# Kernel tuning notes

Measured on AMD Instinct MI355X. Metric: run time of the kernel, lower is better.

Reference implementation:

```python
import jax, jax.numpy as jnp
import numpy as np

NUM_OBJ = 32
OBJ_DIM = 128
MSG_W = 256
FIN_W = 256
BATCH = 256
BN_EPS = 1e-5
NEG_SLOPE = 0.01


def _linear_init(key, fan_in, fan_out):
    # torch nn.Linear default: U(-1/sqrt(fan_in), 1/sqrt(fan_in))
    kw, kb = jax.random.split(key)
    bound = 1.0 / np.sqrt(fan_in)
    w = jax.random.uniform(kw, (fan_out, fan_in), jnp.float32, -bound, bound)
    b = jax.random.uniform(kb, (fan_out,), jnp.float32, -bound, bound)
    return w, b


def setup_inputs() -> dict:
    key = jax.random.key(0)
    ks = jax.random.split(key, 8)
    state = jax.random.normal(ks[0], (BATCH, NUM_OBJ, OBJ_DIM), jnp.float32)
    edges = jax.random.randint(ks[1], (BATCH, NUM_OBJ * NUM_OBJ), 0, 2).astype(jnp.float32)
    msg_w1, msg_b1 = _linear_init(ks[2], OBJ_DIM * 2, MSG_W)
    msg_w2, msg_b2 = _linear_init(ks[3], MSG_W, OBJ_DIM)
    fin_w1, fin_b1 = _linear_init(ks[4], OBJ_DIM * 2, FIN_W)
    fin_w2, fin_b2 = _linear_init(ks[5], FIN_W, OBJ_DIM)
    msg_gamma = jnp.ones((MSG_W,), jnp.float32)
    msg_beta = jnp.zeros((MSG_W,), jnp.float32)
    fin_gamma = jnp.ones((FIN_W,), jnp.float32)
    fin_beta = jnp.zeros((FIN_W,), jnp.float32)
    return {
        "state": state, "edges": edges,
        "msg_w1": msg_w1, "msg_b1": msg_b1, "msg_gamma": msg_gamma, "msg_beta": msg_beta,
        "msg_w2": msg_w2, "msg_b2": msg_b2,
        "fin_w1": fin_w1, "fin_b1": fin_b1, "fin_gamma": fin_gamma, "fin_beta": fin_beta,
        "fin_w2": fin_w2, "fin_b2": fin_b2,
    }


def _batchnorm_train(x, gamma, beta):
    # training-mode BatchNorm1d: batch stats over rows, biased variance
    mean = jnp.mean(x, axis=0)
    var = jnp.mean(jnp.square(x - mean), axis=0)
    return (x - mean) * jax.lax.rsqrt(var + BN_EPS) * gamma + beta


def _mlp(x, w1, b1, gamma, beta, w2, b2):
    h = x @ w1.T + b1
    h = _batchnorm_train(h, gamma, beta)
    h = jnp.where(h >= 0, h, NEG_SLOPE * h)  # LeakyReLU
    return h @ w2.T + b2


def reference(state, edges, msg_w1, msg_b1, msg_gamma, msg_beta, msg_w2, msg_b2,
              fin_w1, fin_b1, fin_gamma, fin_beta, fin_w2, fin_b2):
    B, n, d = state.shape
    src = jnp.repeat(jnp.arange(n), n)   # [n*n]
    tgt = jnp.tile(jnp.arange(n), n)     # [n*n]
    sources = state[:, src]              # [B, n*n, d]
    targets = state[:, tgt]              # [B, n*n, d]
    e = edges[:, :, None]                # [B, n*n, 1]
    need = jnp.concatenate([sources * e, targets * e], axis=2)  # [B, n*n, 2d]
    msgs = _mlp(need.reshape(-1, 2 * d), msg_w1, msg_b1, msg_gamma, msg_beta, msg_w2, msg_b2)
    agg = jnp.sum(msgs.reshape(B, n, n, d), axis=2)  # sum over inner edge group
    sm = jnp.concatenate([state, agg], axis=2).reshape(-1, 2 * d)
    out = _mlp(sm, fin_w1, fin_b1, fin_gamma, fin_beta, fin_w2, fin_b2)
    return out.reshape(B, n, d)
```

## Files before the change

### kernel.cpp

```cpp
#include <hip/hip_runtime.h>

#define NOBJ   32
#define DIM    128
#define HW     256
#define R1     8192
#define NPAIR  262144
#define BN_EPS 1e-5f

typedef unsigned short u16;
typedef unsigned int   u32;
typedef __attribute__((ext_vector_type(8))) short bf16x8;
typedef __attribute__((ext_vector_type(4))) float f32x4;
typedef __attribute__((ext_vector_type(4))) unsigned short u16x4;
typedef __attribute__((ext_vector_type(4))) unsigned int u32x4;

__device__ __forceinline__ u16 f2bf(float f) {
    union { float f; unsigned u; } v; v.f = f;
    unsigned r = v.u + 0x7fffu + ((v.u >> 16) & 1u);
    return (u16)(r >> 16);
}
__device__ __forceinline__ float bf2f(u16 u) {
    union { unsigned u; float f; } v; v.u = ((unsigned)u) << 16; return v.f;
}
__device__ __forceinline__ u16x4 cvt4(float4 v) {
    u16x4 r;
    r[0] = f2bf(v.x); r[1] = f2bf(v.y); r[2] = f2bf(v.z); r[3] = f2bf(v.w);
    return r;
}
__device__ __forceinline__ bf16x8 cvt8_f32(const float* p) {
    f32x4 v0 = *(const f32x4*)p, v1 = *(const f32x4*)(p + 4);
    bf16x8 r;
    #pragma unroll
    for (int k = 0; k < 4; ++k) {
        r[k]     = (short)f2bf(v0[k]);
        r[4 + k] = (short)f2bf(v1[k]);
    }
    return r;
}
__device__ __forceinline__ bf16x8 cvt8_bn(const float* p, const float* a, const float* d) {
    f32x4 v0 = *(const f32x4*)p, v1 = *(const f32x4*)(p + 4);
    f32x4 a0 = *(const f32x4*)a, a1 = *(const f32x4*)(a + 4);
    f32x4 d0 = *(const f32x4*)d, d1 = *(const f32x4*)(d + 4);
    bf16x8 r;
    #pragma unroll
    for (int k = 0; k < 4; ++k) {
        float x0 = fmaf(a0[k], v0[k], d0[k]); x0 = fmaxf(x0, 0.01f * x0);
        float x1 = fmaf(a1[k], v1[k], d1[k]); x1 = fmaxf(x1, 0.01f * x1);
        r[k]     = (short)f2bf(x0);
        r[4 + k] = (short)f2bf(x1);
    }
    return r;
}

__global__ __launch_bounds__(256) void prep_kernel(
    const float* __restrict__ w1, const float4* __restrict__ w2,
    const float4* __restrict__ fw1, const float4* __restrict__ fw2,
    u16x4* __restrict__ W1b, u16x4* __restrict__ W2b,
    u16x4* __restrict__ FW1b, u16x4* __restrict__ FW2b,
    f32x4* __restrict__ sums)
{
    int g = blockIdx.x * 256 + threadIdx.x;
    if (g < 16384) {
        const int o = g * 4, n = o >> 7, k = o & 127;
        const float4 v = *(const float4*)(w1 + (n < 256 ? n * 256 + k
                                                        : (n - 256) * 256 + 128 + k));
        W1b[g] = cvt4(v); return;
    }
    g -= 16384;
    if (g < 8192) { W2b[g] = cvt4(w2[g]); return; }
    g -= 8192;
    if (g < 16384) { FW1b[g] = cvt4(fw1[g]); return; }
    g -= 16384;
    if (g < 8192) { FW2b[g] = cvt4(fw2[g]); return; }
    g -= 8192;
    if (g < 264) { const f32x4 z = {}; sums[g] = z; }
}

__global__ __launch_bounds__(512) void pq_stats(
    const float* __restrict__ state, const u16* __restrict__ W1b,
    const float* __restrict__ edges, const float* __restrict__ b1,
    u16* __restrict__ PQb, u16* __restrict__ Ab, float* __restrict__ EQf,
    float* __restrict__ sums)
{
    __shared__ float Pls[32 * 256];
    __shared__ float Qls[33 * 256];
    __shared__ float redA[8 * 256];
    __shared__ float redB[8 * 256];
    __shared__ u32 masks[32];
    __shared__ __align__(16) unsigned char list8[32 * 32];
    __shared__ float cdf[32];

    const int b    = blockIdx.x;
    const int t    = threadIdx.x;
    const int lane = t & 63;
    const int w    = t >> 6;
    const int lr   = lane & 15;
    const int lk   = (lane >> 4) * 8;
    const int c0   = lane * 4;

    if (t < 256) ((u32*)list8)[t] = 0x20202020u;
    if (t < 64) { const f32x4 z = {}; *(f32x4*)&Qls[32 * 256 + t * 4] = z; }

    const int il_t = t >> 5;
    const int j_t  = t & 31;
    const float ev0 = edges[(size_t)b * 1024 + il_t * 32 + j_t];
    const float ev1 = edges[(size_t)b * 1024 + (il_t + 16) * 32 + j_t];

    const int col0 = w * 64;
    f32x4 acc[2][4] = {};
    #pragma unroll
    for (int ks = 0; ks < 4; ++ks) {
        const int kabs = ks * 32 + lk;
        bf16x8 af[2];
        #pragma unroll
        for (int rf = 0; rf < 2; ++rf)
            af[rf] = cvt8_f32(state + (size_t)(b * 32 + rf * 16 + lr) * 128 + kabs);
        if (w == 0) {
            #pragma unroll
            for (int rf = 0; rf < 2; ++rf)
                *(bf16x8*)(Ab + (size_t)(b * 32 + rf * 16 + lr) * 128 + kabs) = af[rf];
        }
        #pragma unroll
        for (int cf = 0; cf < 4; ++cf) {
            const bf16x8 bf = *(const bf16x8*)(W1b + (size_t)(col0 + cf * 16 + lr) * 128 + kabs);
            #pragma unroll
            for (int rf = 0; rf < 2; ++rf)
                acc[rf][cf] = __builtin_amdgcn_mfma_f32_16x16x32_bf16(af[rf], bf, acc[rf][cf], 0, 0, 0);
        }
    }
    #pragma unroll
    for (int rf = 0; rf < 2; ++rf)
        #pragma unroll
        for (int cf = 0; cf < 4; ++cf) {
            const int col = col0 + cf * 16 + lr;
            #pragma unroll
            for (int r = 0; r < 4; ++r) {
                const int row = rf * 16 + (lane >> 4) * 4 + r;
                const u16 u = f2bf(acc[rf][cf][r]);
                PQb[(size_t)(b * 32 + row) * 512 + col] = u;
                const float fv = bf2f(u);
                if (w < 4) Pls[row * 256 + col]         = fv;
                else       Qls[row * 256 + (col - 256)] = fv;
            }
        }
    __syncthreads();

    {
        const unsigned long long bal0 = __ballot(ev0 != 0.f);
        const u32 m0 = (lane < 32) ? (u32)bal0 : (u32)(bal0 >> 32);
        if (ev0 != 0.f)
            list8[il_t * 32 + __popc(m0 & ((1u << j_t) - 1u))] = (unsigned char)j_t;
        if (j_t == 0) masks[il_t] = m0;
        const unsigned long long bal1 = __ballot(ev1 != 0.f);
        const u32 m1 = (lane < 32) ? (u32)bal1 : (u32)(bal1 >> 32);
        if (ev1 != 0.f)
            list8[(il_t + 16) * 32 + __popc(m1 & ((1u << j_t) - 1u))] = (unsigned char)j_t;
        if (j_t == 0) masks[il_t + 16] = m1;
    }
    __syncthreads();

    if (t < 32) {
        u32 cnt = 0;
        #pragma unroll
        for (int i = 0; i < 32; ++i) cnt += (masks[i] >> t) & 1u;
        cdf[t] = (float)cnt;
    }
    if (t == 0) {
        int tot = 0;
        #pragma unroll
        for (int i = 0; i < 32; ++i) tot += __popc(masks[i]);
        atomicAdd(&sums[512], (float)tot);
    }

    const f32x4 b14 = *(const f32x4*)(b1 + c0);
    f32x4 sumA = {}, sumB = {};

    #pragma unroll
    for (int ii = 0; ii < 4; ++ii) {
        const int il = w * 4 + ii;
        const int n1 = __popc(masks[il]);
        const int npad = (n1 + 3) & ~3;
        const float frd = (float)n1;
        f32x4 eq = {};
        const u32x4 l0 = *(const u32x4*)(list8 + il * 32);
        const u32x4 l1 = *(const u32x4*)(list8 + il * 32 + 16);
        const u32 wbuf[8] = {l0[0], l0[1], l0[2], l0[3], l1[0], l1[1], l1[2], l1[3]};
        #pragma unroll
        for (int wi = 0; wi < 8; ++wi) {
            if (wi * 4 >= npad) break;
            const u32 w4 = wbuf[wi];
            #pragma unroll
            for (int kb = 0; kb < 4; ++kb) {
                const int j = (w4 >> (kb * 8)) & 0xff;
                const f32x4 q = *(const f32x4*)&Qls[j * 256 + c0];
                #pragma unroll
                for (int k = 0; k < 4; ++k) eq[k] += q[k];
            }
        }
        *(f32x4*)(EQf + (size_t)(b * 32 + il) * 256 + c0) = eq;
        const f32x4 p4 = *(const f32x4*)&Pls[il * 256 + c0];
        #pragma unroll
        for (int k = 0; k < 4; ++k) {
            const float pb = p4[k] + b14[k];
            sumA[k] += frd * pb + eq[k];
            sumB[k] = fmaf(frd * pb + 2.f * eq[k], pb, sumB[k]);
        }
    }
    __syncthreads();

    #pragma unroll
    for (int jj = 0; jj < 4; ++jj) {
        const int j = w * 4 + jj;
        const float cdj = cdf[j];
        const f32x4 q = *(const f32x4*)&Qls[j * 256 + c0];
        #pragma unroll
        for (int k = 0; k < 4; ++k) sumB[k] = fmaf(cdj * q[k], q[k], sumB[k]);
    }
    *(f32x4*)&redA[w * 256 + c0] = sumA;
    *(f32x4*)&redB[w * 256 + c0] = sumB;
    __syncthreads();
    if (t < 256) {
        float a = 0.f, bb = 0.f;
        #pragma unroll
        for (int ww = 0; ww < 8; ++ww) {
            a  += redA[ww * 256 + t];
            bb += redB[ww * 256 + t];
        }
        atomicAdd(&sums[t], a);
        atomicAdd(&sums[256 + t], bb);
    }
}

__global__ __launch_bounds__(256) void s_agg_kernel(
    const u16* __restrict__ PQb, const float* __restrict__ edges,
    const float* __restrict__ EQf, const float* __restrict__ sums,
    const float* __restrict__ gamma, const float* __restrict__ beta,
    const float* __restrict__ b1,
    const u16* __restrict__ W2b, const float* __restrict__ b2,
    u16* __restrict__ aggb)
{
    __shared__ float Qls[33 * 256];
    __shared__ u16 Ssb[16 * 256];
    __shared__ __align__(16) unsigned char list8[16 * 32];
    __shared__ int n1s[16];

    const int b    = blockIdx.x;
    const int i0   = blockIdx.y * 16;
    const int t    = threadIdx.x;
    const int lane = t & 63;
    const int w    = t >> 6;
    const int lr   = lane & 15;
    const int lk   = (lane >> 4) * 8;
    const int c0   = lane * 4;

    const float Etot = sums[512];
    const float nz   = (float)NPAIR - Etot;
    const float invN = 1.f / (float)NPAIR;
    const f32x4 s1  = *(const f32x4*)(sums + c0);
    const f32x4 s2  = *(const f32x4*)(sums + 256 + c0);
    const f32x4 g4  = *(const f32x4*)(gamma + c0);
    const f32x4 be4 = *(const f32x4*)(beta + c0);
    const f32x4 b14 = *(const f32x4*)(b1 + c0);
    f32x4 a4, d4, ld4;
    #pragma unroll
    for (int k = 0; k < 4; ++k) {
        const float mean = (s1[k] + nz * b14[k]) * invN;
        const float ms   = (s2[k] + nz * b14[k] * b14[k]) * invN;
        const float var  = fmaf(-mean, mean, ms);
        a4[k]  = g4[k] * rsqrtf(var + BN_EPS);
        d4[k]  = fmaf(b14[k] - mean, a4[k], be4[k]);
        ld4[k] = fmaxf(d4[k], 0.01f * d4[k]);
    }

    #pragma unroll
    for (int it = 0; it < 8; ++it) {
        const int row = w + it * 4;
        const u16x4 qu = *(const u16x4*)(PQb + (size_t)(b * 32 + row) * 512 + 256 + c0);
        f32x4 q;
        #pragma unroll
        for (int k = 0; k < 4; ++k) q[k] = a4[k] * bf2f(qu[k]);
        *(f32x4*)&Qls[row * 256 + c0] = q;
    }
    if (t < 64) { const f32x4 z = {}; *(f32x4*)&Qls[32 * 256 + t * 4] = z; }
    if (t < 128) ((u32*)list8)[t] = 0x20202020u;

    const int il_t = t >> 5;
    const int j_t  = t & 31;
    const float ev0 = edges[(size_t)b * 1024 + (i0 + il_t) * 32 + j_t];
    const float ev1 = edges[(size_t)b * 1024 + (i0 + 8 + il_t) * 32 + j_t];
    __syncthreads();

    {
        const unsigned long long bal0 = __ballot(ev0 != 0.f);
        const u32 m0 = (lane < 32) ? (u32)bal0 : (u32)(bal0 >> 32);
        if (ev0 != 0.f)
            list8[il_t * 32 + __popc(m0 & ((1u << j_t) - 1u))] = (unsigned char)j_t;
        if (j_t == 0) n1s[il_t] = __popc(m0);
        const unsigned long long bal1 = __ballot(ev1 != 0.f);
        const u32 m1 = (lane < 32) ? (u32)bal1 : (u32)(bal1 >> 32);
        if (ev1 != 0.f)
            list8[(8 + il_t) * 32 + __popc(m1 & ((1u << j_t) - 1u))] = (unsigned char)j_t;
        if (j_t == 0) n1s[8 + il_t] = __popc(m1);
    }
    __syncthreads();

    #pragma unroll
    for (int ii = 0; ii < 4; ++ii) {
        const int il = 4 * w + ii;
        const int gi = b * 32 + i0 + il;
        const int n1 = n1s[il];
        const int npad = (n1 + 3) & ~3;
        const float frd = (float)n1;
        const float fz = (float)(32 - n1);
        const float fp = (float)(npad - n1);
        const u16x4 pu = *(const u16x4*)(PQb + (size_t)gi * 512 + c0);
        const f32x4 eq4 = *(const f32x4*)(EQf + (size_t)gi * 256 + c0);
        f32x4 ap, absacc;
        #pragma unroll
        for (int k = 0; k < 4; ++k) {
            ap[k] = fmaf(a4[k], bf2f(pu[k]), d4[k]);
            absacc[k] = -fp * fabsf(ap[k]);
        }
        const u32x4 l0 = *(const u32x4*)(list8 + il * 32);
        const u32x4 l1 = *(const u32x4*)(list8 + il * 32 + 16);
        const u32 wbuf[8] = {l0[0], l0[1], l0[2], l0[3], l1[0], l1[1], l1[2], l1[3]};
        #pragma unroll
        for (int wi = 0; wi < 8; ++wi) {
            if (wi * 4 >= npad) break;
            const u32 w4 = wbuf[wi];
            #pragma unroll
            for (int kb = 0; kb < 4; ++kb) {
                const int j = (w4 >> (kb * 8)) & 0xff;
                const f32x4 q = *(const f32x4*)&Qls[j * 256 + c0];
                #pragma unroll
                for (int k = 0; k < 4; ++k)
                    absacc[k] += fabsf(ap[k] + q[k]);
            }
        }
        u16x4 o;
        #pragma unroll
        for (int k = 0; k < 4; ++k) {
            const float lin = fmaf(frd, ap[k], a4[k] * eq4[k]);
            const float S = fmaf(fz, ld4[k], fmaf(0.505f, lin, 0.495f * absacc[k]));
            o[k] = f2bf(S);
        }
        const int off = (lane * 8) ^ ((il & 7) << 4);
        *(u16x4*)((char*)Ssb + il * 512 + off) = o;
    }
    __syncthreads();

    const int colw = w * 32;
    f32x4 acc2[2] = {};
    #pragma unroll
    for (int ks = 0; ks < 8; ++ks) {
        const int rdoff = (ks * 64 + (lane >> 4) * 16) ^ ((lr & 7) << 4);
        const bf16x8 afr = *(const bf16x8*)((const char*)Ssb + lr * 512 + rdoff);
        #pragma unroll
        for (int cf = 0; cf < 2; ++cf) {
            const bf16x8 bfr = *(const bf16x8*)(W2b + (size_t)(colw + cf * 16 + lr) * 256 + ks * 32 + lk);
            acc2[cf] = __builtin_amdgcn_mfma_f32_16x16x32_bf16(afr, bfr, acc2[cf], 0, 0, 0);
        }
    }
    #pragma unroll
    for (int cf = 0; cf < 2; ++cf) {
        const int col = colw + cf * 16 + lr;
        const float bv = (float)NOBJ * b2[col];
        #pragma unroll
        for (int r = 0; r < 4; ++r) {
            const int rowl = (lane >> 4) * 4 + r;
            aggb[(size_t)(b * 32 + i0 + rowl) * 128 + col] = f2bf(acc2[cf][r] + bv);
        }
    }
}

__global__ __launch_bounds__(256) void h2_gemm(
    const u16* __restrict__ Ab, const u16* __restrict__ aggb,
    const u16* __restrict__ FW1b, const float* __restrict__ fb1,
    float* __restrict__ H2, float* __restrict__ sums2)
{
    __shared__ float sred[64];
    const int lane = threadIdx.x & 63;
    const int wave = threadIdx.x >> 6;
    const int row0 = blockIdx.y * 64 + wave * 16;
    const int col0 = blockIdx.x * 32;
    const int lr = lane & 15;
    const int lk = (lane >> 4) * 8;

    f32x4 acc[2] = {};
    #pragma unroll
    for (int ks = 0; ks < 8; ++ks) {
        const int kabs = ks * 32 + lk;
        const bf16x8 af = (kabs < 128)
            ? *(const bf16x8*)(Ab   + (size_t)(row0 + lr) * 128 + kabs)
            : *(const bf16x8*)(aggb + (size_t)(row0 + lr) * 128 + (kabs - 128));
        #pragma unroll
        for (int cf = 0; cf < 2; ++cf) {
            const bf16x8 bf = *(const bf16x8*)(FW1b + (size_t)(col0 + cf * 16 + lr) * 256 + kabs);
            acc[cf] = __builtin_amdgcn_mfma_f32_16x16x32_bf16(af, bf, acc[cf], 0, 0, 0);
        }
    }

    if (threadIdx.x < 64) sred[threadIdx.x] = 0.f;
    __syncthreads();
    #pragma unroll
    for (int cf = 0; cf < 2; ++cf) {
        const int col = col0 + cf * 16 + lr;
        const float bv = fb1[col];
        float s = 0.f, ss = 0.f;
        #pragma unroll
        for (int r = 0; r < 4; ++r) {
            const int row = row0 + (lane >> 4) * 4 + r;
            const float v = acc[cf][r] + bv;
            H2[(size_t)row * 256 + col] = v;
            s += v;
            ss = fmaf(v, v, ss);
        }
        atomicAdd(&sred[cf * 16 + lr], s);
        atomicAdd(&sred[32 + cf * 16 + lr], ss);
    }
    __syncthreads();
    if (threadIdx.x < 32) {
        atomicAdd(&sums2[col0 + threadIdx.x], sred[threadIdx.x]);
        atomicAdd(&sums2[256 + col0 + threadIdx.x], sred[32 + threadIdx.x]);
    }
}

__global__ __launch_bounds__(256) void out_gemm(
    const float* __restrict__ H2, const u16* __restrict__ FW2b,
    const float* __restrict__ fb2, const float* __restrict__ sums2,
    const float* __restrict__ gamma, const float* __restrict__ beta,
    float* __restrict__ out)
{
    __shared__ float adl[512];
    const int t = threadIdx.x;
    {
        const float invN = 1.f / (float)R1;
        const float mean = sums2[t] * invN;
        const float var  = fmaf(-mean, mean, sums2[256 + t] * invN);
        const float a    = gamma[t] * rsqrtf(var + BN_EPS);
        adl[t]       = a;
        adl[256 + t] = fmaf(-mean, a, beta[t]);
    }
    __syncthreads();

    const int lane = t & 63;
    const int wave = t >> 6;
    const int row0 = blockIdx.y * 64 + wave * 16;
    const int col0 = blockIdx.x * 32;
    const int lr = lane & 15;
    const int lk = (lane >> 4) * 8;

    f32x4 acc[2] = {};
    #pragma unroll
    for (int ks = 0; ks < 8; ++ks) {
        const int kabs = ks * 32 + lk;
        const bf16x8 af = cvt8_bn(H2 + (size_t)(row0 + lr) * 256 + kabs,
                                  adl + kabs, adl + 256 + kabs);
        #pragma unroll
        for (int cf = 0; cf < 2; ++cf) {
            const bf16x8 bf = *(const bf16x8*)(FW2b + (size_t)(col0 + cf * 16 + lr) * 256 + kabs);
            acc[cf] = __builtin_amdgcn_mfma_f32_16x16x32_bf16(af, bf, acc[cf], 0, 0, 0);
        }
    }
    #pragma unroll
    for (int cf = 0; cf < 2; ++cf) {
        const int col = col0 + cf * 16 + lr;
        const float bv = fb2[col];
        #pragma unroll
        for (int r = 0; r < 4; ++r) {
            const int row = row0 + (lane >> 4) * 4 + r;
            out[(size_t)row * 128 + col] = acc[cf][r] + bv;
        }
    }
}

extern "C" void kernel_launch(void* const* d_in, const int* in_sizes, int n_in,
                              void* d_out, int out_size, void* d_ws, size_t ws_size,
                              hipStream_t stream)
{
    const float* state     = (const float*)d_in[0];
    const float* edges     = (const float*)d_in[1];
    const float* msg_w1    = (const float*)d_in[2];
    const float* msg_b1    = (const float*)d_in[3];
    const float* msg_gamma = (const float*)d_in[4];
    const float* msg_beta  = (const float*)d_in[5];
    const float* msg_w2    = (const float*)d_in[6];
    const float* msg_b2    = (const float*)d_in[7];
    const float* fin_w1    = (const float*)d_in[8];
    const float* fin_b1    = (const float*)d_in[9];
    const float* fin_gamma = (const float*)d_in[10];
    const float* fin_beta  = (const float*)d_in[11];
    const float* fin_w2    = (const float*)d_in[12];
    const float* fin_b2    = (const float*)d_in[13];

    char* w = (char*)d_ws;
    u16*   PQb  = (u16*)(w);
    u16*   Ab   = (u16*)(w + 8388608);
    u16*   aggb = (u16*)(w + 10485760);
    float* H2   = (float*)(w + 12582912);
    float* EQf  = (float*)(w + 20971520);
    u16*   W1b  = (u16*)(w + 29360128);
    u16*   W2b  = (u16*)(w + 29491200);
    u16*   FW1b = (u16*)(w + 29556736);
    u16*   FW2b = (u16*)(w + 29687808);
    float* sums = (float*)(w + 29753344);
    float* sums2 = sums + 544;

    prep_kernel<<<195, 256, 0, stream>>>(
        msg_w1, (const float4*)msg_w2, (const float4*)fin_w1, (const float4*)fin_w2,
        (u16x4*)W1b, (u16x4*)W2b, (u16x4*)FW1b, (u16x4*)FW2b, (f32x4*)sums);

    pq_stats<<<256, 512, 0, stream>>>(state, W1b, edges, msg_b1,
                                      PQb, Ab, EQf, sums);

    s_agg_kernel<<<dim3(256, 2), 256, 0, stream>>>(
        PQb, edges, EQf, sums, msg_gamma, msg_beta, msg_b1, W2b, msg_b2, aggb);

    h2_gemm<<<dim3(8, 128), 256, 0, stream>>>(Ab, aggb, FW1b, fin_b1, H2, sums2);

    out_gemm<<<dim3(4, 128), 256, 0, stream>>>(
        H2, FW2b, fin_b2, sums2, fin_gamma, fin_beta, (float*)d_out);
}
```

Baseline: 69.39 us.

## Fuse four pipeline kernels into one persistent kernel with grid barriers

Merges pq_stats, s_agg, h2_gemm and out_gemm into a single 256-block persistent kernel. Intermediates (P/Q, state bf16, agg, H2) now stay in LDS, and the two global BatchNorm reductions are handled by software grid barriers built on atomics. This removes kernel launch gaps and the global-memory round trips for PQ, EQ, agg and H2. In exchange it relies on all 256 blocks being co-resident, which risks deadlock if they are not, and it uses a large LDS footprint per block. Each block now performs its batch's full work, so the s_agg split over two row halves is lost.

```diff
diff --git a/kernel.cpp b/kernel.cpp
--- a/kernel.cpp
+++ b/kernel.cpp
@@ -1,11 +1,8 @@
 #include <hip/hip_runtime.h>
 
-#define NOBJ   32
-#define DIM    128
-#define HW     256
-#define R1     8192
 #define NPAIR  262144
 #define BN_EPS 1e-5f
+#define NBLK   256
 
 typedef unsigned short u16;
 typedef unsigned int   u32;
@@ -37,19 +34,35 @@
     }
     return r;
 }
-__device__ __forceinline__ bf16x8 cvt8_bn(const float* p, const float* a, const float* d) {
-    f32x4 v0 = *(const f32x4*)p, v1 = *(const f32x4*)(p + 4);
+__device__ __forceinline__ bf16x8 cvt8_bn_lds(const u16* p, const float* a, const float* d) {
+    u16x4 v0 = *(const u16x4*)p, v1 = *(const u16x4*)(p + 4);
     f32x4 a0 = *(const f32x4*)a, a1 = *(const f32x4*)(a + 4);
     f32x4 d0 = *(const f32x4*)d, d1 = *(const f32x4*)(d + 4);
     bf16x8 r;
     #pragma unroll
     for (int k = 0; k < 4; ++k) {
-        float x0 = fmaf(a0[k], v0[k], d0[k]); x0 = fmaxf(x0, 0.01f * x0);
-        float x1 = fmaf(a1[k], v1[k], d1[k]); x1 = fmaxf(x1, 0.01f * x1);
+        float x0 = fmaf(a0[k], bf2f(v0[k]), d0[k]); x0 = fmaxf(x0, 0.01f * x0);
+        float x1 = fmaf(a1[k], bf2f(v1[k]), d1[k]); x1 = fmaxf(x1, 0.01f * x1);
         r[k]     = (short)f2bf(x0);
         r[4 + k] = (short)f2bf(x1);
     }
     return r;
+}
+
+__device__ __forceinline__ void gridbar(u32* cnt, u32* gen) {
+    __syncthreads();
+    __threadfence();
+    if (threadIdx.x == 0) {
+        const u32 g = __hip_atomic_load(gen, __ATOMIC_ACQUIRE, __HIP_MEMORY_SCOPE_AGENT);
+        const u32 old = __hip_atomic_fetch_add(cnt, 1, __ATOMIC_ACQ_REL, __HIP_MEMORY_SCOPE_AGENT);
+        if (old == NBLK - 1) {
+            __hip_atomic_store(cnt, 0, __ATOMIC_RELEASE, __HIP_MEMORY_SCOPE_AGENT);
+            __hip_atomic_fetch_add(gen, 1, __ATOMIC_ACQ_REL, __HIP_MEMORY_SCOPE_AGENT);
+        } else {
+            while (__hip_atomic_load(gen, __ATOMIC_ACQUIRE, __HIP_MEMORY_SCOPE_AGENT) == g) {}
+        }
+    }
+    __syncthreads();
 }
 
 __global__ __launch_bounds__(256) void prep_kernel(
@@ -57,7 +70,7 @@
     const float4* __restrict__ fw1, const float4* __restrict__ fw2,
     u16x4* __restrict__ W1b, u16x4* __restrict__ W2b,
     u16x4* __restrict__ FW1b, u16x4* __restrict__ FW2b,
-    f32x4* __restrict__ sums)
+    f32x4* __restrict__ sums4, u32* __restrict__ bar)
 {
     int g = blockIdx.x * 256 + threadIdx.x;
     if (g < 16384) {
@@ -67,95 +80,105 @@
         W1b[g] = cvt4(v); return;
     }
     g -= 16384;
-    if (g < 8192) { W2b[g] = cvt4(w2[g]); return; }
+    if (g < 8192)  { W2b[g]  = cvt4(w2[g]);  return; }
     g -= 8192;
     if (g < 16384) { FW1b[g] = cvt4(fw1[g]); return; }
     g -= 16384;
-    if (g < 8192) { FW2b[g] = cvt4(fw2[g]); return; }
+    if (g < 8192)  { FW2b[g] = cvt4(fw2[g]); return; }
     g -= 8192;
-    if (g < 264) { const f32x4 z = {}; sums[g] = z; }
-}
-
-__global__ __launch_bounds__(512) void pq_stats(
-    const float* __restrict__ state, const u16* __restrict__ W1b,
-    const float* __restrict__ edges, const float* __restrict__ b1,
-    u16* __restrict__ PQb, u16* __restrict__ Ab, float* __restrict__ EQf,
-    float* __restrict__ sums)
+    if (g < 272)   { const f32x4 z = {}; sums4[g] = z; return; }
+    if (g == 272)  { bar[0] = 0; bar[1] = 0; bar[2] = 0; bar[3] = 0; }
+}
+
+__global__ __launch_bounds__(512, 2) void mega_kernel(
+    const float* __restrict__ state, const float* __restrict__ edges,
+    const float* __restrict__ b1, const float* __restrict__ g1,
+    const float* __restrict__ be1, const float* __restrict__ b2,
+    const float* __restrict__ fb1, const float* __restrict__ g2,
+    const float* __restrict__ be2, const float* __restrict__ fb2,
+    const u16* __restrict__ W1b, const u16* __restrict__ W2b,
+    const u16* __restrict__ FW1b, const u16* __restrict__ FW2b,
+    float* __restrict__ sums, u32* __restrict__ bar,
+    float* __restrict__ out)
 {
-    __shared__ float Pls[32 * 256];
-    __shared__ float Qls[33 * 256];
-    __shared__ float redA[8 * 256];
-    __shared__ float redB[8 * 256];
+    __shared__ float Pf[32 * 256];
+    __shared__ float Qf[33 * 256];
+    __shared__ u16 Asb[32 * 128];
+    __shared__ __align__(16) char pool[24576];
+    __shared__ u16 H2s[32 * 256];
+    __shared__ __align__(16) unsigned char list8[32 * 32];
     __shared__ u32 masks[32];
-    __shared__ __align__(16) unsigned char list8[32 * 32];
     __shared__ float cdf[32];
+    __shared__ float sred[512];
+    __shared__ float adl[512];
 
     const int b    = blockIdx.x;
     const int t    = threadIdx.x;
     const int lane = t & 63;
     const int w    = t >> 6;
     const int lr   = lane & 15;
-    const int lk   = (lane >> 4) * 8;
+    const int lkg  = lane >> 4;
+    const int lk   = lkg * 8;
     const int c0   = lane * 4;
 
     if (t < 256) ((u32*)list8)[t] = 0x20202020u;
-    if (t < 64) { const f32x4 z = {}; *(f32x4*)&Qls[32 * 256 + t * 4] = z; }
-
-    const int il_t = t >> 5;
-    const int j_t  = t & 31;
-    const float ev0 = edges[(size_t)b * 1024 + il_t * 32 + j_t];
-    const float ev1 = edges[(size_t)b * 1024 + (il_t + 16) * 32 + j_t];
-
-    const int col0 = w * 64;
-    f32x4 acc[2][4] = {};
-    #pragma unroll
-    for (int ks = 0; ks < 4; ++ks) {
-        const int kabs = ks * 32 + lk;
-        bf16x8 af[2];
+    if (t < 64) { const f32x4 z = {}; *(f32x4*)&Qf[32 * 256 + t * 4] = z; }
+
+    const int il0 = t >> 5;
+    const int jt  = t & 31;
+    const float ev0 = edges[(size_t)b * 1024 + il0 * 32 + jt];
+    const float ev1 = edges[(size_t)b * 1024 + (il0 + 16) * 32 + jt];
+
+    {
+        const int col0 = w * 64;
+        f32x4 acc[2][4] = {};
+        #pragma unroll
+        for (int ks = 0; ks < 4; ++ks) {
+            const int kabs = ks * 32 + lk;
+            bf16x8 af[2];
+            #pragma unroll
+            for (int rf = 0; rf < 2; ++rf) {
+                af[rf] = cvt8_f32(state + (size_t)(b * 32 + rf * 16 + lr) * 128 + kabs);
+                if (w == 0) {
+                    const int row = rf * 16 + lr;
+                    *(bf16x8*)((char*)Asb + ((row * 256 + kabs * 2) ^ ((row & 7) << 4))) = af[rf];
+                }
+            }
+            #pragma unroll
+            for (int cf = 0; cf < 4; ++cf) {
+                const bf16x8 bfr = *(const bf16x8*)(W1b + (size_t)(col0 + cf * 16 + lr) * 128 + kabs);
+                #pragma unroll
+                for (int rf = 0; rf < 2; ++rf)
+                    acc[rf][cf] = __builtin_amdgcn_mfma_f32_16x16x32_bf16(af[rf], bfr, acc[rf][cf], 0, 0, 0);
+            }
+        }
         #pragma unroll
         for (int rf = 0; rf < 2; ++rf)
-            af[rf] = cvt8_f32(state + (size_t)(b * 32 + rf * 16 + lr) * 128 + kabs);
-        if (w == 0) {
-            #pragma unroll
-            for (int rf = 0; rf < 2; ++rf)
-                *(bf16x8*)(Ab + (size_t)(b * 32 + rf * 16 + lr) * 128 + kabs) = af[rf];
-        }
-        #pragma unroll
-        for (int cf = 0; cf < 4; ++cf) {
-            const bf16x8 bf = *(const bf16x8*)(W1b + (size_t)(col0 + cf * 16 + lr) * 128 + kabs);
-            #pragma unroll
-            for (int rf = 0; rf < 2; ++rf)
-                acc[rf][cf] = __builtin_amdgcn_mfma_f32_16x16x32_bf16(af[rf], bf, acc[rf][cf], 0, 0, 0);
-        }
-    }
-    #pragma unroll
-    for (int rf = 0; rf < 2; ++rf)
-        #pragma unroll
-        for (int cf = 0; cf < 4; ++cf) {
-            const int col = col0 + cf * 16 + lr;
-            #pragma unroll
-            for (int r = 0; r < 4; ++r) {
-                const int row = rf * 16 + (lane >> 4) * 4 + r;
-                const u16 u = f2bf(acc[rf][cf][r]);
-                PQb[(size_t)(b * 32 + row) * 512 + col] = u;
-                const float fv = bf2f(u);
-                if (w < 4) Pls[row * 256 + col]         = fv;
-                else       Qls[row * 256 + (col - 256)] = fv;
-            }
-        }
+            #pragma unroll
+            for (int cf = 0; cf < 4; ++cf) {
+                const int col = col0 + cf * 16 + lr;
+                #pragma unroll
+                for (int r = 0; r < 4; ++r) {
+                    const int row = rf * 16 + lkg * 4 + r;
+                    const float v = acc[rf][cf][r];
+                    if (col < 256) Pf[row * 256 + col] = v;
+                    else           Qf[row * 256 + (col - 256)] = v;
+                }
+            }
+    }
     __syncthreads();
 
     {
         const unsigned long long bal0 = __ballot(ev0 != 0.f);
         const u32 m0 = (lane < 32) ? (u32)bal0 : (u32)(bal0 >> 32);
         if (ev0 != 0.f)
-            list8[il_t * 32 + __popc(m0 & ((1u << j_t) - 1u))] = (unsigned char)j_t;
-        if (j_t == 0) masks[il_t] = m0;
+            list8[il0 * 32 + __popc(m0 & ((1u << jt) - 1u))] = (unsigned char)jt;
+        if (jt == 0) masks[il0] = m0;
         const unsigned long long bal1 = __ballot(ev1 != 0.f);
         const u32 m1 = (lane < 32) ? (u32)bal1 : (u32)(bal1 >> 32);
         if (ev1 != 0.f)
-            list8[(il_t + 16) * 32 + __popc(m1 & ((1u << j_t) - 1u))] = (unsigned char)j_t;
-        if (j_t == 0) masks[il_t + 16] = m1;
+            list8[(il0 + 16) * 32 + __popc(m1 & ((1u << jt) - 1u))] = (unsigned char)jt;
+        if (jt == 0) masks[il0 + 16] = m1;
     }
     __syncthreads();
 
@@ -173,14 +196,14 @@
     }
 
     const f32x4 b14 = *(const f32x4*)(b1 + c0);
+    f32x4 eqr[4];
     f32x4 sumA = {}, sumB = {};
 
     #pragma unroll
     for (int ii = 0; ii < 4; ++ii) {
-        const int il = w * 4 + ii;
+        const int il = 4 * w + ii;
         const int n1 = __popc(masks[il]);
         const int npad = (n1 + 3) & ~3;
-        const float frd = (float)n1;
         f32x4 eq = {};
         const u32x4 l0 = *(const u32x4*)(list8 + il * 32);
         const u32x4 l1 = *(const u32x4*)(list8 + il * 32 + 16);
@@ -192,13 +215,14 @@
             #pragma unroll
             for (int kb = 0; kb < 4; ++kb) {
                 const int j = (w4 >> (kb * 8)) & 0xff;
-                const f32x4 q = *(const f32x4*)&Qls[j * 256 + c0];
+                const f32x4 q = *(const f32x4*)&Qf[j * 256 + c0];
                 #pragma unroll
                 for (int k = 0; k < 4; ++k) eq[k] += q[k];
             }
         }
-        *(f32x4*)(EQf + (size_t)(b * 32 + il) * 256 + c0) = eq;
-        const f32x4 p4 = *(const f32x4*)&Pls[il * 256 + c0];
+        eqr[ii] = eq;
+        const f32x4 p4 = *(const f32x4*)&Pf[il * 256 + c0];
+        const float frd = (float)n1;
         #pragma unroll
         for (int k = 0; k < 4; ++k) {
             const float pb = p4[k] + b14[k];
@@ -208,64 +232,49 @@
     }
     __syncthreads();
 
-    #pragma unroll
-    for (int jj = 0; jj < 4; ++jj) {
-        const int j = w * 4 + jj;
-        const float cdj = cdf[j];
-        const f32x4 q = *(const f32x4*)&Qls[j * 256 + c0];
-        #pragma unroll
-        for (int k = 0; k < 4; ++k) sumB[k] = fmaf(cdj * q[k], q[k], sumB[k]);
-    }
-    *(f32x4*)&redA[w * 256 + c0] = sumA;
-    *(f32x4*)&redB[w * 256 + c0] = sumB;
-    __syncthreads();
-    if (t < 256) {
-        float a = 0.f, bb = 0.f;
-        #pragma unroll
-        for (int ww = 0; ww < 8; ++ww) {
-            a  += redA[ww * 256 + t];
-            bb += redB[ww * 256 + t];
-        }
-        atomicAdd(&sums[t], a);
-        atomicAdd(&sums[256 + t], bb);
-    }
-}
-
-__global__ __launch_bounds__(256) void s_agg_kernel(
-    const u16* __restrict__ PQb, const float* __restrict__ edges,
-    const float* __restrict__ EQf, const float* __restrict__ sums,
-    const float* __restrict__ gamma, const float* __restrict__ beta,
-    const float* __restrict__ b1,
-    const u16* __restrict__ W2b, const float* __restrict__ b2,
-    u16* __restrict__ aggb)
-{
-    __shared__ float Qls[33 * 256];
-    __shared__ u16 Ssb[16 * 256];
-    __shared__ __align__(16) unsigned char list8[16 * 32];
-    __shared__ int n1s[16];
-
-    const int b    = blockIdx.x;
-    const int i0   = blockIdx.y * 16;
-    const int t    = threadIdx.x;
-    const int lane = t & 63;
-    const int w    = t >> 6;
-    const int lr   = lane & 15;
-    const int lk   = (lane >> 4) * 8;
-    const int c0   = lane * 4;
+    {
+        float* redA = (float*)pool;
+        float* redB = (float*)pool + 2048;
+        #pragma unroll
+        for (int jj = 0; jj < 4; ++jj) {
+            const int j = 4 * w + jj;
+            const float cdj = cdf[j];
+            const f32x4 q = *(const f32x4*)&Qf[j * 256 + c0];
+            #pragma unroll
+            for (int k = 0; k < 4; ++k) sumB[k] = fmaf(cdj * q[k], q[k], sumB[k]);
+        }
+        *(f32x4*)&redA[w * 256 + c0] = sumA;
+        *(f32x4*)&redB[w * 256 + c0] = sumB;
+        __syncthreads();
+        if (t < 256) {
+            float a = 0.f, bb = 0.f;
+            #pragma unroll
+            for (int ww = 0; ww < 8; ++ww) {
+                a  += redA[ww * 256 + t];
+                bb += redB[ww * 256 + t];
+            }
+            atomicAdd(&sums[t], a);
+            atomicAdd(&sums[256 + t], bb);
+        }
+    }
+
+    gridbar(&bar[0], &bar[1]);
+
+    u16* Ssb  = (u16*)pool;
+    u16* aggs = (u16*)(pool + 16384);
 
     const float Etot = sums[512];
-    const float nz   = (float)NPAIR - Etot;
+    const float nzc  = (float)NPAIR - Etot;
     const float invN = 1.f / (float)NPAIR;
     const f32x4 s1  = *(const f32x4*)(sums + c0);
     const f32x4 s2  = *(const f32x4*)(sums + 256 + c0);
-    const f32x4 g4  = *(const f32x4*)(gamma + c0);
-    const f32x4 be4 = *(const f32x4*)(beta + c0);
-    const f32x4 b14 = *(const f32x4*)(b1 + c0);
+    const f32x4 g4  = *(const f32x4*)(g1 + c0);
+    const f32x4 be4 = *(const f32x4*)(be1 + c0);
     f32x4 a4, d4, ld4;
     #pragma unroll
     for (int k = 0; k < 4; ++k) {
-        const float mean = (s1[k] + nz * b14[k]) * invN;
-        const float ms   = (s2[k] + nz * b14[k] * b14[k]) * invN;
+        const float mean = (s1[k] + nzc * b14[k]) * invN;
+        const float ms   = (s2[k] + nzc * b14[k] * b14[k]) * invN;
         const float var  = fmaf(-mean, mean, ms);
         a4[k]  = g4[k] * rsqrtf(var + BN_EPS);
         d4[k]  = fmaf(b14[k] - mean, a4[k], be4[k]);
@@ -273,52 +282,18 @@
     }
 
     #pragma unroll
-    for (int it = 0; it < 8; ++it) {
-        const int row = w + it * 4;
-        const u16x4 qu = *(const u16x4*)(PQb + (size_t)(b * 32 + row) * 512 + 256 + c0);
-        f32x4 q;
-        #pragma unroll
-        for (int k = 0; k < 4; ++k) q[k] = a4[k] * bf2f(qu[k]);
-        *(f32x4*)&Qls[row * 256 + c0] = q;
-    }
-    if (t < 64) { const f32x4 z = {}; *(f32x4*)&Qls[32 * 256 + t * 4] = z; }
-    if (t < 128) ((u32*)list8)[t] = 0x20202020u;
-
-    const int il_t = t >> 5;
-    const int j_t  = t & 31;
-    const float ev0 = edges[(size_t)b * 1024 + (i0 + il_t) * 32 + j_t];
-    const float ev1 = edges[(size_t)b * 1024 + (i0 + 8 + il_t) * 32 + j_t];
-    __syncthreads();
-
-    {
-        const unsigned long long bal0 = __ballot(ev0 != 0.f);
-        const u32 m0 = (lane < 32) ? (u32)bal0 : (u32)(bal0 >> 32);
-        if (ev0 != 0.f)
-            list8[il_t * 32 + __popc(m0 & ((1u << j_t) - 1u))] = (unsigned char)j_t;
-        if (j_t == 0) n1s[il_t] = __popc(m0);
-        const unsigned long long bal1 = __ballot(ev1 != 0.f);
-        const u32 m1 = (lane < 32) ? (u32)bal1 : (u32)(bal1 >> 32);
-        if (ev1 != 0.f)
-            list8[(8 + il_t) * 32 + __popc(m1 & ((1u << j_t) - 1u))] = (unsigned char)j_t;
-        if (j_t == 0) n1s[8 + il_t] = __popc(m1);
-    }
-    __syncthreads();
-
-    #pragma unroll
     for (int ii = 0; ii < 4; ++ii) {
         const int il = 4 * w + ii;
-        const int gi = b * 32 + i0 + il;
-        const int n1 = n1s[il];
+        const int n1 = __popc(masks[il]);
         const int npad = (n1 + 3) & ~3;
         const float frd = (float)n1;
-        const float fz = (float)(32 - n1);
-        const float fp = (float)(npad - n1);
-        const u16x4 pu = *(const u16x4*)(PQb + (size_t)gi * 512 + c0);
-        const f32x4 eq4 = *(const f32x4*)(EQf + (size_t)gi * 256 + c0);
+        const float fz  = (float)(32 - n1);
+        const float fp  = (float)(npad - n1);
+        const f32x4 p4 = *(const f32x4*)&Pf[il * 256 + c0];
         f32x4 ap, absacc;
         #pragma unroll
         for (int k = 0; k < 4; ++k) {
-            ap[k] = fmaf(a4[k], bf2f(pu[k]), d4[k]);
+            ap[k] = fmaf(a4[k], p4[k], d4[k]);
             absacc[k] = -fp * fabsf(ap[k]);
         }
         const u32x4 l0 = *(const u32x4*)(list8 + il * 32);
@@ -331,146 +306,131 @@
             #pragma unroll
             for (int kb = 0; kb < 4; ++kb) {
                 const int j = (w4 >> (kb * 8)) & 0xff;
-                const f32x4 q = *(const f32x4*)&Qls[j * 256 + c0];
+                const f32x4 q = *(const f32x4*)&Qf[j * 256 + c0];
                 #pragma unroll
                 for (int k = 0; k < 4; ++k)
-                    absacc[k] += fabsf(ap[k] + q[k]);
+                    absacc[k] += fabsf(fmaf(a4[k], q[k], ap[k]));
             }
         }
         u16x4 o;
         #pragma unroll
         for (int k = 0; k < 4; ++k) {
-            const float lin = fmaf(frd, ap[k], a4[k] * eq4[k]);
+            const float lin = fmaf(frd, ap[k], a4[k] * eqr[ii][k]);
             const float S = fmaf(fz, ld4[k], fmaf(0.505f, lin, 0.495f * absacc[k]));
             o[k] = f2bf(S);
         }
-        const int off = (lane * 8) ^ ((il & 7) << 4);
-        *(u16x4*)((char*)Ssb + il * 512 + off) = o;
-    }
-    __syncthreads();
-
-    const int colw = w * 32;
-    f32x4 acc2[2] = {};
-    #pragma unroll
-    for (int ks = 0; ks < 8; ++ks) {
-        const int rdoff = (ks * 64 + (lane >> 4) * 16) ^ ((lr & 7) << 4);
-        const bf16x8 afr = *(const bf16x8*)((const char*)Ssb + lr * 512 + rdoff);
+        *(u16x4*)((char*)Ssb + il * 512 + ((lane * 8) ^ ((il & 7) << 4))) = o;
+    }
+    __syncthreads();
+
+    {
+        f32x4 acc2[2] = {};
+        #pragma unroll
+        for (int ks = 0; ks < 8; ++ks) {
+            const bf16x8 bfr = *(const bf16x8*)(W2b + (size_t)(w * 16 + lr) * 256 + ks * 32 + lk);
+            const int rdoff = ks * 64 + lkg * 16;
+            #pragma unroll
+            for (int rf = 0; rf < 2; ++rf) {
+                const int row = rf * 16 + lr;
+                const bf16x8 afr = *(const bf16x8*)((char*)Ssb + row * 512 + (rdoff ^ ((row & 7) << 4)));
+                acc2[rf] = __builtin_amdgcn_mfma_f32_16x16x32_bf16(afr, bfr, acc2[rf], 0, 0, 0);
+            }
+        }
+        const int col = w * 16 + lr;
+        const float bv = 32.f * b2[col];
+        #pragma unroll
+        for (int rf = 0; rf < 2; ++rf)
+            #pragma unroll
+            for (int r = 0; r < 4; ++r) {
+                const int row = rf * 16 + lkg * 4 + r;
+                *(u16*)((char*)aggs + ((row * 256 + col * 2) ^ ((row & 7) << 4))) = f2bf(acc2[rf][r] + bv);
+            }
+    }
+    sred[t] = 0.f;
+    __syncthreads();
+
+    {
+        f32x4 acc3[2][2] = {};
+        #pragma unroll
+        for (int ks = 0; ks < 8; ++ks) {
+            const int kabs = ks * 32 + lk;
+            bf16x8 af3[2];
+            #pragma unroll
+            for (int rf = 0; rf < 2; ++rf) {
+                const int row = rf * 16 + lr;
+                if (ks < 4)
+                    af3[rf] = *(const bf16x8*)((char*)Asb + ((row * 256 + kabs * 2) ^ ((row & 7) << 4)));
+                else
+                    af3[rf] = *(const bf16x8*)((char*)aggs + ((row * 256 + (kabs - 128) * 2) ^ ((row & 7) << 4)));
+            }
+            #pragma unroll
+            for (int cf = 0; cf < 2; ++cf) {
+                const bf16x8 bfr = *(const bf16x8*)(FW1b + (size_t)(w * 32 + cf * 16 + lr) * 256 + kabs);
+                #pragma unroll
+                for (int rf = 0; rf < 2; ++rf)
+                    acc3[rf][cf] = __builtin_amdgcn_mfma_f32_16x16x32_bf16(af3[rf], bfr, acc3[rf][cf], 0, 0, 0);
+            }
+        }
         #pragma unroll
         for (int cf = 0; cf < 2; ++cf) {
-            const bf16x8 bfr = *(const bf16x8*)(W2b + (size_t)(colw + cf * 16 + lr) * 256 + ks * 32 + lk);
-            acc2[cf] = __builtin_amdgcn_mfma_f32_16x16x32_bf16(afr, bfr, acc2[cf], 0, 0, 0);
-        }
-    }
-    #pragma unroll
-    for (int cf = 0; cf < 2; ++cf) {
-        const int col = colw + cf * 16 + lr;
-        const float bv = (float)NOBJ * b2[col];
-        #pragma unroll
-        for (int r = 0; r < 4; ++r) {
-            const int rowl = (lane >> 4) * 4 + r;
-            aggb[(size_t)(b * 32 + i0 + rowl) * 128 + col] = f2bf(acc2[cf][r] + bv);
-        }
-    }
-}
-
-__global__ __launch_bounds__(256) void h2_gemm(
-    const u16* __restrict__ Ab, const u16* __restrict__ aggb,
-    const u16* __restrict__ FW1b, const float* __restrict__ fb1,
-    float* __restrict__ H2, float* __restrict__ sums2)
-{
-    __shared__ float sred[64];
-    const int lane = threadIdx.x & 63;
-    const int wave = threadIdx.x >> 6;
-    const int row0 = blockIdx.y * 64 + wave * 16;
-    const int col0 = blockIdx.x * 32;
-    const int lr = lane & 15;
-    const int lk = (lane >> 4) * 8;
-
-    f32x4 acc[2] = {};
-    #pragma unroll
-    for (int ks = 0; ks < 8; ++ks) {
-        const int kabs = ks * 32 + lk;
-        const bf16x8 af = (kabs < 128)
-            ? *(const bf16x8*)(Ab   + (size_t)(row0 + lr) * 128 + kabs)
-            : *(const bf16x8*)(aggb + (size_t)(row0 + lr) * 128 + (kabs - 128));
-        #pragma unroll
-        for (int cf = 0; cf < 2; ++cf) {
-            const bf16x8 bf = *(const bf16x8*)(FW1b + (size_t)(col0 + cf * 16 + lr) * 256 + kabs);
-            acc[cf] = __builtin_amdgcn_mfma_f32_16x16x32_bf16(af, bf, acc[cf], 0, 0, 0);
-        }
-    }
-
-    if (threadIdx.x < 64) sred[threadIdx.x] = 0.f;
-    __syncthreads();
-    #pragma unroll
-    for (int cf = 0; cf < 2; ++cf) {
-        const int col = col0 + cf * 16 + lr;
-        const float bv = fb1[col];
-        float s = 0.f, ss = 0.f;
-        #pragma unroll
-        for (int r = 0; r < 4; ++r) {
-            const int row = row0 + (lane >> 4) * 4 + r;
-            const float v = acc[cf][r] + bv;
-            H2[(size_t)row * 256 + col] = v;
-            s += v;
-            ss = fmaf(v, v, ss);
-        }
-        atomicAdd(&sred[cf * 16 + lr], s);
-        atomicAdd(&sred[32 + cf * 16 + lr], ss);
-    }
-    __syncthreads();
-    if (threadIdx.x < 32) {
-        atomicAdd(&sums2[col0 + threadIdx.x], sred[threadIdx.x]);
-        atomicAdd(&sums2[256 + col0 + threadIdx.x], sred[32 + threadIdx.x]);
-    }
-}
-
-__global__ __launch_bounds__(256) void out_gemm(
-    const float* __restrict__ H2, const u16* __restrict__ FW2b,
-    const float* __restrict__ fb2, const float* __restrict__ sums2,
-    const float* __restrict__ gamma, const float* __restrict__ beta,
-    float* __restrict__ out)
-{
-    __shared__ float adl[512];
-    const int t = threadIdx.x;
-    {
-        const float invN = 1.f / (float)R1;
-        const float mean = sums2[t] * invN;
-        const float var  = fmaf(-mean, mean, sums2[256 + t] * invN);
-        const float a    = gamma[t] * rsqrtf(var + BN_EPS);
+            const int col = w * 32 + cf * 16 + lr;
+            const float bv = fb1[col];
+            float s = 0.f, ss = 0.f;
+            #pragma unroll
+            for (int rf = 0; rf < 2; ++rf)
+                #pragma unroll
+                for (int r = 0; r < 4; ++r) {
+                    const int row = rf * 16 + lkg * 4 + r;
+                    const float v = acc3[rf][cf][r] + bv;
+                    *(u16*)((char*)H2s + ((row * 512 + col * 2) ^ ((row & 7) << 4))) = f2bf(v);
+                    s += v;
+                    ss = fmaf(v, v, ss);
+                }
+            atomicAdd(&sred[col], s);
+            atomicAdd(&sred[256 + col], ss);
+        }
+    }
+    __syncthreads();
+    if (t < 256) {
+        atomicAdd(&sums[544 + t], sred[t]);
+        atomicAdd(&sums[544 + 256 + t], sred[256 + t]);
+    }
+
+    gridbar(&bar[2], &bar[3]);
+
+    if (t < 256) {
+        const float invR = 1.f / 8192.f;
+        const float mean = sums[544 + t] * invR;
+        const float var  = fmaf(-mean, mean, sums[544 + 256 + t] * invR);
+        const float a    = g2[t] * rsqrtf(var + BN_EPS);
         adl[t]       = a;
-        adl[256 + t] = fmaf(-mean, a, beta[t]);
-    }
-    __syncthreads();
-
-    const int lane = t & 63;
-    const int wave = t >> 6;
-    const int row0 = blockIdx.y * 64 + wave * 16;
-    const int col0 = blockIdx.x * 32;
-    const int lr = lane & 15;
-    const int lk = (lane >> 4) * 8;
-
-    f32x4 acc[2] = {};
-    #pragma unroll
-    for (int ks = 0; ks < 8; ++ks) {
-        const int kabs = ks * 32 + lk;
-        const bf16x8 af = cvt8_bn(H2 + (size_t)(row0 + lr) * 256 + kabs,
-                                  adl + kabs, adl + 256 + kabs);
-        #pragma unroll
-        for (int cf = 0; cf < 2; ++cf) {
-            const bf16x8 bf = *(const bf16x8*)(FW2b + (size_t)(col0 + cf * 16 + lr) * 256 + kabs);
-            acc[cf] = __builtin_amdgcn_mfma_f32_16x16x32_bf16(af, bf, acc[cf], 0, 0, 0);
-        }
-    }
-    #pragma unroll
-    for (int cf = 0; cf < 2; ++cf) {
-        const int col = col0 + cf * 16 + lr;
+        adl[256 + t] = fmaf(-mean, a, be2[t]);
+    }
+    __syncthreads();
+
+    {
+        f32x4 acc4[2] = {};
+        #pragma unroll
+        for (int ks = 0; ks < 8; ++ks) {
+            const int kabs = ks * 32 + lk;
+            const bf16x8 bfr = *(const bf16x8*)(FW2b + (size_t)(w * 16 + lr) * 256 + kabs);
+            #pragma unroll
+            for (int rf = 0; rf < 2; ++rf) {
+                const int row = rf * 16 + lr;
+                const u16* hp = (const u16*)((char*)H2s + ((row * 512 + kabs * 2) ^ ((row & 7) << 4)));
+                const bf16x8 af4 = cvt8_bn_lds(hp, adl + kabs, adl + 256 + kabs);
+                acc4[rf] = __builtin_amdgcn_mfma_f32_16x16x32_bf16(af4, bfr, acc4[rf], 0, 0, 0);
+            }
+        }
+        const int col = w * 16 + lr;
         const float bv = fb2[col];
         #pragma unroll
-        for (int r = 0; r < 4; ++r) {
-            const int row = row0 + (lane >> 4) * 4 + r;
-            out[(size_t)row * 128 + col] = acc[cf][r] + bv;
-        }
+        for (int rf = 0; rf < 2; ++rf)
+            #pragma unroll
+            for (int r = 0; r < 4; ++r) {
+                const int row = rf * 16 + lkg * 4 + r;
+                out[(size_t)(b * 32 + row) * 128 + col] = acc4[rf][r] + bv;
+            }
     }
 }
 
@@ -494,30 +454,20 @@
     const float* fin_b2    = (const float*)d_in[13];
 
     char* w = (char*)d_ws;
-    u16*   PQb  = (u16*)(w);
-    u16*   Ab   = (u16*)(w + 8388608);
-    u16*   aggb = (u16*)(w + 10485760);
-    float* H2   = (float*)(w + 12582912);
-    float* EQf  = (float*)(w + 20971520);
-    u16*   W1b  = (u16*)(w + 29360128);
-    u16*   W2b  = (u16*)(w + 29491200);
-    u16*   FW1b = (u16*)(w + 29556736);
-    u16*   FW2b = (u16*)(w + 29687808);
-    float* sums = (float*)(w + 29753344);
-    float* sums2 = sums + 544;
-
-    prep_kernel<<<195, 256, 0, stream>>>(
+    u16*   W1b  = (u16*)(w);
+    u16*   W2b  = (u16*)(w + 131072);
+    u16*   FW1b = (u16*)(w + 196608);
+    u16*   FW2b = (u16*)(w + 327680);
+    float* sums = (float*)(w + 393216);
+    u32*   bar  = (u32*)(w + 397568);
+
+    prep_kernel<<<256, 256, 0, stream>>>(
         msg_w1, (const float4*)msg_w2, (const float4*)fin_w1, (const float4*)fin_w2,
-        (u16x4*)W1b, (u16x4*)W2b, (u16x4*)FW1b, (u16x4*)FW2b, (f32x4*)sums);
-
-    pq_stats<<<256, 512, 0, stream>>>(state, W1b, edges, msg_b1,
-                                      PQb, Ab, EQf, sums);
-
-    s_agg_kernel<<<dim3(256, 2), 256, 0, stream>>>(
-        PQb, edges, EQf, sums, msg_gamma, msg_beta, msg_b1, W2b, msg_b2, aggb);
-
-    h2_gemm<<<dim3(8, 128), 256, 0, stream>>>(Ab, aggb, FW1b, fin_b1, H2, sums2);
-
-    out_gemm<<<dim3(4, 128), 256, 0, stream>>>(
-        H2, FW2b, fin_b2, sums2, fin_gamma, fin_beta, (float*)d_out);
-}
+        (u16x4*)W1b, (u16x4*)W2b, (u16x4*)FW1b, (u16x4*)FW2b,
+        (f32x4*)sums, bar);
+
+    mega_kernel<<<NBLK, 512, 0, stream>>>(
+        state, edges, msg_b1, msg_gamma, msg_beta, msg_b2,
+        fin_b1, fin_gamma, fin_beta, fin_b2,
+        W1b, W2b, FW1b, FW2b, sums, bar, (float*)d_out);
+}
```

After: 153.7 us. 2.22x slower.
